# Kernel optimization log

Measured on AMD Instinct MI355X. Metric: run time of the kernel, lower is better.

The kernel has to match this reference:

```python
import jax, jax.numpy as jnp
import numpy as np

B, IN, H = 8192, 1024, 1024
WRANK, UR0, UR1, G = 256, 64, 32, 2
HG = H // G


def setup_inputs() -> dict:
    key = jax.random.key(0)
    ks = jax.random.split(key, 24)
    r = lambda k, shp: 0.1 * jax.random.normal(k, shp, dtype=jnp.float32)
    inp = {
        "x": jax.random.normal(ks[0], (B, IN), dtype=jnp.float32),
        "h": jax.random.normal(ks[1], (B, H), dtype=jnp.float32),
        "c": jax.random.normal(ks[2], (B, H), dtype=jnp.float32),
        "W": r(ks[3], (IN, WRANK)),
        "W1": r(ks[4], (WRANK, H)),
        "W2": r(ks[5], (WRANK, H)),
        "W3": r(ks[6], (WRANK, H)),
        "W4": r(ks[7], (WRANK, H)),
        "U": r(ks[8], (G, HG, UR0)),
        "U1": r(ks[9], (G, UR0, HG)),
        "U2": r(ks[10], (G, UR0, HG)),
        "U3": r(ks[11], (G, UR0, HG)),
        "U4": r(ks[12], (G, UR0, HG)),
        "UU": r(ks[13], (G, HG, UR1)),
        "UU1": r(ks[14], (G, UR1, HG)),
        "UU2": r(ks[15], (G, UR1, HG)),
        "UU3": r(ks[16], (G, UR1, HG)),
        "UU4": r(ks[17], (G, UR1, HG)),
        "bias_f": jnp.ones((1, H), dtype=jnp.float32),
        "bias_i": jnp.ones((1, H), dtype=jnp.float32),
        "bias_c": jnp.ones((1, H), dtype=jnp.float32),
        "bias_o": jnp.ones((1, H), dtype=jnp.float32),
    }
    return inp


def _grouped(hg, Ushare, Ui):
    # hg: [B, g, hg]; Ushare: [g, hg, r]; Ui: [g, r, hg] -> [B, H]
    t = jnp.einsum('bgd,gdr->bgr', hg, Ushare)
    return jnp.einsum('bgr,grd->bgd', t, Ui).reshape(hg.shape[0], H)


def reference(x, h, c, W, W1, W2, W3, W4, U, U1, U2, U3, U4,
              UU, UU1, UU2, UU3, UU4, bias_f, bias_i, bias_c, bias_o):
    # low-rank W path
    xw = x @ W                      # [B, wRank]
    wVal1, wVal2, wVal3, wVal4 = xw @ W1, xw @ W2, xw @ W3, xw @ W4

    # grouped low-rank U path (diagonal groups)
    hg = h.reshape(B, G, HG)
    tU = jnp.einsum('bgd,gdr->bgr', hg, U)          # shared projection
    uVal1 = jnp.einsum('bgr,grd->bgd', tU, U1).reshape(B, H)
    uVal2 = jnp.einsum('bgr,grd->bgd', tU, U2).reshape(B, H)
    uVal3 = jnp.einsum('bgr,grd->bgd', tU, U3).reshape(B, H)
    uVal4 = jnp.einsum('bgr,grd->bgd', tU, U4).reshape(B, H)

    # grouped UU path on group-rotated h (index = [1..g-1, 0])
    hg3 = jnp.roll(hg, -1, axis=1)
    tUU = jnp.einsum('bgd,gdr->bgr', hg3, UU)
    uuVal1 = jnp.einsum('bgr,grd->bgd', tUU, UU1).reshape(B, H)
    uuVal2 = jnp.einsum('bgr,grd->bgd', tUU, UU2).reshape(B, H)
    uuVal3 = jnp.einsum('bgr,grd->bgd', tUU, UU3).reshape(B, H)
    uuVal4 = jnp.einsum('bgr,grd->bgd', tUU, UU4).reshape(B, H)

    matVal_i = wVal1 + uVal1 + uuVal1
    matVal_f = wVal2 + uVal2 + uuVal2
    matVal_o = wVal3 + uVal3 + uuVal3
    matVal_c = wVal4 + uVal4 + uuVal4

    i = jax.nn.sigmoid(matVal_i + bias_i)
    f = jax.nn.sigmoid(matVal_f + bias_f)
    o = jax.nn.sigmoid(matVal_o + bias_o)
    c_tilda = jnp.tanh(matVal_c + bias_c)

    c_next = f * c + i * c_tilda
    h_next = o * jnp.tanh(c_next)
    return (c_next, h_next)
```

## Files before the change

kernel.cpp:

```cpp
#include <hip/hip_runtime.h>
#include <hip/hip_bf16.h>

#define B_ROWS 8192
#define IN_DIM 1024
#define H_DIM  1024
#define WRANK  256
#define UR0    64
#define UR1    32
#define HGD    512
#define KTOT   384
#define A2_LD  512

typedef __attribute__((ext_vector_type(8))) short bf16x8;
typedef __attribute__((ext_vector_type(4))) float f32x4;
typedef __attribute__((ext_vector_type(4))) float float4v;

__device__ __forceinline__ unsigned short f2bf(float f) {
    union { float f; unsigned u; } v; v.f = f;
    unsigned r = v.u + 0x7FFF + ((v.u >> 16) & 1);
    return (unsigned short)(r >> 16);
}

__device__ __forceinline__ void gld16(void* lds, const void* g) {
    __builtin_amdgcn_global_load_lds(
        (const __attribute__((address_space(1))) unsigned int*)g,
        (__attribute__((address_space(3))) unsigned int*)lds, 16, 0, 0);
}

__device__ __forceinline__ float fsig(float x)  { return 1.f / (1.f + __expf(-x)); }
__device__ __forceinline__ float ftanh(float x) { return 1.f - 2.f / (__expf(2.f * x) + 1.f); }

__global__ __launch_bounds__(256)
void pack_weights(const float* __restrict__ W,
                  const float* __restrict__ W1, const float* __restrict__ W2,
                  const float* __restrict__ W3, const float* __restrict__ W4,
                  const float* __restrict__ U,  const float* __restrict__ U1,
                  const float* __restrict__ U2, const float* __restrict__ U3,
                  const float* __restrict__ U4,
                  const float* __restrict__ UU, const float* __restrict__ UU1,
                  const float* __restrict__ UU2,const float* __restrict__ UU3,
                  const float* __restrict__ UU4,
                  unsigned short* __restrict__ WbfT,
                  unsigned short* __restrict__ HPbf,
                  unsigned short* __restrict__ GateBT)
{
    const float* Wg[4]  = {W1, W2, W3, W4};
    const float* Ug[4]  = {U1, U2, U3, U4};
    const float* UUg[4] = {UU1, UU2, UU3, UU4};
    const long N_WT = 256L * 1024;
    const long N_HP = 256L * 512;
    const long N_GB = 4L * 1024 * KTOT;
    const long total = N_WT + N_HP + N_GB;
    for (long t = blockIdx.x * 256L + threadIdx.x; t < total; t += (long)gridDim.x * 256L) {
        if (t < N_WT) {
            int n = (int)(t >> 10), p = (int)(t & 1023);
            int span = p >> 6, slp = (p >> 3) & 7, e = p & 7;
            int k = span * 64 + ((slp ^ (n & 7)) << 3) + e;
            WbfT[t] = f2bf(W[(size_t)k * WRANK + n]);
        } else if (t < N_WT + N_HP) {
            long u = t - N_WT;
            int n = (int)(u >> 9), p = (int)(u & 511);
            int span = p >> 6, slp = (p >> 3) & 7, e = p & 7;
            int k = span * 64 + ((slp ^ (n & 7)) << 3) + e;
            float v;
            if (n < 64)       v = U [(size_t)k * UR0 + n];
            else if (n < 96)  v = UU[(size_t)(HGD + k) * UR1 + (n - 64)];
            else if (n < 128) v = 0.f;
            else if (n < 192) v = U [(size_t)(HGD + k) * UR0 + (n - 128)];
            else if (n < 224) v = UU[(size_t)k * UR1 + (n - 192)];
            else              v = 0.f;
            HPbf[u] = f2bf(v);
        } else {
            long u = t - N_WT - N_HP;
            int q = (int)(u / (1024L * KTOT));
            long w = u - (long)q * 1024 * KTOT;
            int n = (int)(w / KTOT), p = (int)(w % KTOT);
            int span = p >> 6, slp = (p >> 3) & 7, e = p & 7;
            int k = span * 64 + ((slp ^ (n & 7)) << 3) + e;
            int g = n >> 9, nn = n & 511;
            float v;
            if (k < WRANK)            v = Wg[q][(size_t)k * H_DIM + n];
            else if (k < WRANK + UR0) v = Ug[q][((size_t)g * UR0 + (k - WRANK)) * HGD + nn];
            else if (k < 352)         v = UUg[q][((size_t)g * UR1 + (k - 320)) * HGD + nn];
            else                      v = 0.f;
            GateBT[u] = f2bf(v);
        }
    }
}

__global__ __launch_bounds__(256, 2)
void s1_kernel(const float* __restrict__ x, const float* __restrict__ h,
               const unsigned short* __restrict__ WbfT,
               const unsigned short* __restrict__ HPbf,
               unsigned short* __restrict__ A2)
{
    __shared__ short As[128 * 64];
    __shared__ short Bs[64 * 64];

    const int flat = blockIdx.x;
    const int id = (flat & 7) * 64 + (flat >> 3);
    const int bx = id & 7, by = id >> 3;
    const int m0 = by * 128;

    const bool pa = bx < 4;
    const int Kdim = pa ? IN_DIM : HGD;
    const float* Af = pa ? x : h;
    const int a_off = pa ? 0 : ((bx - 4) >> 1) * HGD;
    const unsigned short* Bw = pa ? (WbfT + (size_t)(bx * 64) * IN_DIM)
                                  : (HPbf + (size_t)((bx - 4) * 64) * HGD);
    const int ldbw = pa ? IN_DIM : HGD;
    const int ccol0 = pa ? bx * 64 : WRANK + (bx - 4) * 64;

    const int tid = threadIdx.x, lane = tid & 63, wid = tid >> 6;
    const int wr = wid >> 1, wc = wid & 1;
    const int lr = lane & 15, lh = lane >> 4;

    f32x4 acc[4][2];
    #pragma unroll
    for (int i = 0; i < 4; ++i)
        #pragma unroll
        for (int j = 0; j < 2; ++j) acc[i][j] = (f32x4){0.f, 0.f, 0.f, 0.f};

    for (int k0 = 0; k0 < Kdim; k0 += 64) {
        #pragma unroll
        for (int t = 0; t < 2; ++t) {
            int u = wid + t * 4;
            const char* src = (const char*)Bw
                + ((size_t)(u * 8 + (lane >> 3)) * ldbw + k0) * 2 + (lane & 7) * 16;
            gld16((char*)Bs + u * 1024, src);
        }
        #pragma unroll
        for (int t = 0; t < 4; ++t) {
            int c = tid + t * 256;
            int row = c >> 3, slot = c & 7;
            const float* p = Af + (size_t)(m0 + row) * 1024 + a_off + k0 + slot * 8;
            float4v f0 = *(const float4v*)p, f1 = *(const float4v*)(p + 4);
            union { bf16x8 v; unsigned short s[8]; } uv;
            uv.s[0] = f2bf(f0.x); uv.s[1] = f2bf(f0.y);
            uv.s[2] = f2bf(f0.z); uv.s[3] = f2bf(f0.w);
            uv.s[4] = f2bf(f1.x); uv.s[5] = f2bf(f1.y);
            uv.s[6] = f2bf(f1.z); uv.s[7] = f2bf(f1.w);
            *(bf16x8*)((char*)As + row * 128 + ((slot ^ (row & 7)) << 4)) = uv.v;
        }
        __syncthreads();
        #pragma unroll
        for (int ks = 0; ks < 2; ++ks) {
            bf16x8 af[4];
            #pragma unroll
            for (int i = 0; i < 4; ++i) {
                int r = wr * 64 + i * 16 + lr;
                af[i] = *(const bf16x8*)((const char*)As + r * 128 + (((ks * 4 + lh) ^ (r & 7)) << 4));
            }
            #pragma unroll
            for (int j = 0; j < 2; ++j) {
                int r = wc * 32 + j * 16 + lr;
                bf16x8 rb = *(const bf16x8*)((const char*)Bs + r * 128 + (((ks * 4 + lh) ^ (r & 7)) << 4));
                #pragma unroll
                for (int i = 0; i < 4; ++i)
                    acc[i][j] = __builtin_amdgcn_mfma_f32_16x16x32_bf16(af[i], rb, acc[i][j], 0, 0, 0);
            }
        }
        __syncthreads();
    }

    #pragma unroll
    for (int i = 0; i < 4; ++i) {
        #pragma unroll
        for (int j = 0; j < 2; ++j) {
            int ncol = ccol0 + wc * 32 + j * 16 + lr;
            int span = ncol >> 6, sl = (ncol >> 3) & 7, e = ncol & 7;
            #pragma unroll
            for (int rr = 0; rr < 4; ++rr) {
                int brow = m0 + wr * 64 + i * 16 + lh * 4 + rr;
                int phys = span * 64 + ((sl ^ (brow & 7)) << 3) + e;
                A2[(size_t)brow * A2_LD + phys] = f2bf(acc[i][j][rr]);
            }
        }
    }
}

__global__ __launch_bounds__(512, 2)
void s2_kernel(const unsigned short* __restrict__ A2,
               const unsigned short* __restrict__ GateBT,
               const float* __restrict__ bias_f, const float* __restrict__ bias_i,
               const float* __restrict__ bias_c, const float* __restrict__ bias_o,
               const float* __restrict__ cin,
               float* __restrict__ cout, float* __restrict__ hout)
{
    __shared__ short As[2][256 * 64];
    __shared__ short Bs[2][4][64 * 64];

    const int flat = blockIdx.x;
    const int id = (flat & 7) * 64 + (flat >> 3);
    const int nt = id & 15, mt = id >> 4;
    const int m0 = mt * 256, n0 = nt * 64, g = n0 >> 9;

    const int tid = threadIdx.x, lane = tid & 63, wid = tid >> 6;
    const int wr = wid >> 1, wc = wid & 1;
    const int lr = lane & 15, lh = lane >> 4;
    const int l8 = lane >> 3, l7 = lane & 7;

    f32x4 acc[4][4][2];
    #pragma unroll
    for (int q = 0; q < 4; ++q)
        #pragma unroll
        for (int i = 0; i < 4; ++i)
            #pragma unroll
            for (int j = 0; j < 2; ++j) acc[q][i][j] = (f32x4){0.f, 0.f, 0.f, 0.f};

#define STAGE_S2(buf, s) do {                                                        \
    const int _ms = ((s) < 4) ? (s) : (((s) == 4) ? 4 + 2 * g : 5 + 2 * (g ^ 1));    \
    _Pragma("unroll")                                                                \
    for (int t = 0; t < 4; ++t) {                                                    \
        int u = wid * 4 + t;                                                         \
        gld16((char*)&As[buf][0] + u * 1024,                                         \
              (const char*)A2 + ((size_t)(m0 + u * 8 + l8) * A2_LD + _ms * 64) * 2   \
              + l7 * 16);                                                            \
    }                                                                                \
    _Pragma("unroll")                                                                \
    for (int t = 0; t < 4; ++t) {                                                    \
        int v = wid * 4 + t, q = v >> 3, uu = v & 7;                                 \
        gld16((char*)&Bs[buf][q][0] + uu * 1024,                                     \
              (const char*)GateBT + ((size_t)(q * 1024 + n0 + uu * 8 + l8) * KTOT    \
              + (s) * 64) * 2 + l7 * 16);                                            \
    } } while (0)

    STAGE_S2(0, 0);

    #pragma unroll
    for (int s = 0; s < 6; ++s) {
        const int cur = s & 1;
        if (s < 5) {
            STAGE_S2(cur ^ 1, s + 1);
            asm volatile("s_waitcnt vmcnt(8)" ::: "memory");
        } else {
            asm volatile("s_waitcnt vmcnt(0)" ::: "memory");
        }
        __builtin_amdgcn_s_barrier();
        asm volatile("" ::: "memory");
        __builtin_amdgcn_s_setprio(1);
        #pragma unroll
        for (int ks = 0; ks < 2; ++ks) {
            bf16x8 af[4];
            #pragma unroll
            for (int i = 0; i < 4; ++i) {
                int r = wr * 64 + i * 16 + lr;
                af[i] = *(const bf16x8*)((const char*)&As[cur][0] + r * 128
                        + (((ks * 4 + lh) ^ (r & 7)) << 4));
            }
            #pragma unroll
            for (int q = 0; q < 4; ++q) {
                #pragma unroll
                for (int j = 0; j < 2; ++j) {
                    int r = wc * 32 + j * 16 + lr;
                    bf16x8 rb = *(const bf16x8*)((const char*)&Bs[cur][q][0] + r * 128
                                + (((ks * 4 + lh) ^ (r & 7)) << 4));
                    #pragma unroll
                    for (int i = 0; i < 4; ++i)
                        acc[q][i][j] = __builtin_amdgcn_mfma_f32_16x16x32_bf16(
                            af[i], rb, acc[q][i][j], 0, 0, 0);
                }
            }
        }
        __builtin_amdgcn_s_setprio(0);
        asm volatile("" ::: "memory");
        __builtin_amdgcn_s_barrier();
        asm volatile("" ::: "memory");
    }
#undef STAGE_S2

    #pragma unroll
    for (int j = 0; j < 2; ++j) {
        int ncol = n0 + wc * 32 + j * 16 + lr;
        float Bi = bias_i[ncol], Bf = bias_f[ncol];
        float Bo = bias_o[ncol], Bc = bias_c[ncol];
        #pragma unroll
        for (int i = 0; i < 4; ++i) {
            #pragma unroll
            for (int rr = 0; rr < 4; ++rr) {
                int brow = m0 + wr * 64 + i * 16 + lh * 4 + rr;
                float mi = acc[0][i][j][rr] + Bi;
                float mf = acc[1][i][j][rr] + Bf;
                float mo = acc[2][i][j][rr] + Bo;
                float mc = acc[3][i][j][rr] + Bc;
                float iv = fsig(mi), fv = fsig(mf), ov = fsig(mo);
                float ct = ftanh(mc);
                float cv = cin[(size_t)brow * H_DIM + ncol];
                float cn = fv * cv + iv * ct;
                float hn = ov * ftanh(cn);
                cout[(size_t)brow * H_DIM + ncol] = cn;
                hout[(size_t)brow * H_DIM + ncol] = hn;
            }
        }
    }
}

extern "C" void kernel_launch(void* const* d_in, const int* in_sizes, int n_in,
                              void* d_out, int out_size, void* d_ws, size_t ws_size,
                              hipStream_t stream)
{
    const float* x   = (const float*)d_in[0];
    const float* h   = (const float*)d_in[1];
    const float* c   = (const float*)d_in[2];
    const float* W   = (const float*)d_in[3];
    const float* W1  = (const float*)d_in[4];
    const float* W2  = (const float*)d_in[5];
    const float* W3  = (const float*)d_in[6];
    const float* W4  = (const float*)d_in[7];
    const float* U   = (const float*)d_in[8];
    const float* U1  = (const float*)d_in[9];
    const float* U2  = (const float*)d_in[10];
    const float* U3  = (const float*)d_in[11];
    const float* U4  = (const float*)d_in[12];
    const float* UU  = (const float*)d_in[13];
    const float* UU1 = (const float*)d_in[14];
    const float* UU2 = (const float*)d_in[15];
    const float* UU3 = (const float*)d_in[16];
    const float* UU4 = (const float*)d_in[17];
    const float* bias_f = (const float*)d_in[18];
    const float* bias_i = (const float*)d_in[19];
    const float* bias_c = (const float*)d_in[20];
    const float* bias_o = (const float*)d_in[21];

    unsigned short* A2     = (unsigned short*)d_ws;
    unsigned short* WbfT   = A2   + (size_t)B_ROWS * A2_LD;
    unsigned short* HPbf   = WbfT + 256L * 1024;
    unsigned short* GateBT = HPbf + 256L * 512;

    float* c_out = (float*)d_out;
    float* h_out = c_out + (size_t)B_ROWS * H_DIM;

    pack_weights<<<dim3(2048), dim3(256), 0, stream>>>(
        W, W1, W2, W3, W4, U, U1, U2, U3, U4, UU, UU1, UU2, UU3, UU4,
        WbfT, HPbf, GateBT);

    s1_kernel<<<dim3(512), dim3(256), 0, stream>>>(x, h, WbfT, HPbf, A2);

    s2_kernel<<<dim3(512), dim3(512), 0, stream>>>(
        A2, GateBT, bias_f, bias_i, bias_c, bias_o, c, c_out, h_out);
}
```

Baseline: 94.00 us.

## Retile both GEMM stages with pre-tiled intermediate layouts and pipelined loads

Stage one now uses 64-row tiles with double-buffered B loads and register-prefetched A, and writes its output in a tiled per-slab layout that drops the unused zero-padding columns. Stage two reads 32-wide K slabs from pre-tiled A and gate weight images, so each wave copies contiguous 1KB chunks with no swizzle math. The K depth shrinks from 384 padded to 352, and tile sizes drop so twice as many blocks run with higher occupancy. The cost is more blocks, more barriers per unit of K, and more complex index mapping that is easy to get wrong.

```diff
diff --git a/kernel.cpp b/kernel.cpp
--- a/kernel.cpp
+++ b/kernel.cpp
@@ -8,8 +8,9 @@
 #define UR0    64
 #define UR1    32
 #define HGD    512
-#define KTOT   384
-#define A2_LD  512
+
+#define NS2    11
+#define NTA    14
 
 typedef __attribute__((ext_vector_type(8))) short bf16x8;
 typedef __attribute__((ext_vector_type(4))) float f32x4;
@@ -42,15 +43,15 @@
                   const float* __restrict__ UU4,
                   unsigned short* __restrict__ WbfT,
                   unsigned short* __restrict__ HPbf,
-                  unsigned short* __restrict__ GateBT)
+                  unsigned short* __restrict__ BT2)
 {
     const float* Wg[4]  = {W1, W2, W3, W4};
     const float* Ug[4]  = {U1, U2, U3, U4};
     const float* UUg[4] = {UU1, UU2, UU3, UU4};
     const long N_WT = 256L * 1024;
     const long N_HP = 256L * 512;
-    const long N_GB = 4L * 1024 * KTOT;
-    const long total = N_WT + N_HP + N_GB;
+    const long N_BT = 16L * NS2 * 8192;
+    const long total = N_WT + N_HP + N_BT;
     for (long t = blockIdx.x * 256L + threadIdx.x; t < total; t += (long)gridDim.x * 256L) {
         if (t < N_WT) {
             int n = (int)(t >> 10), p = (int)(t & 1023);
@@ -72,35 +73,34 @@
             HPbf[u] = f2bf(v);
         } else {
             long u = t - N_WT - N_HP;
-            int q = (int)(u / (1024L * KTOT));
-            long w = u - (long)q * 1024 * KTOT;
-            int n = (int)(w / KTOT), p = (int)(w % KTOT);
-            int span = p >> 6, slp = (p >> 3) & 7, e = p & 7;
-            int k = span * 64 + ((slp ^ (n & 7)) << 3) + e;
-            int g = n >> 9, nn = n & 511;
+            int img = (int)(u >> 13);
+            int nt = img / NS2, s = img % NS2;
+            int r = (int)(u & 8191);
+            int q = r >> 11, kc = (r >> 9) & 3, row = (r >> 3) & 63, e = r & 7;
+            int n = nt * 64 + row, g = n >> 9, nn = n & 511;
+            int kk = kc * 8 + e;
             float v;
-            if (k < WRANK)            v = Wg[q][(size_t)k * H_DIM + n];
-            else if (k < WRANK + UR0) v = Ug[q][((size_t)g * UR0 + (k - WRANK)) * HGD + nn];
-            else if (k < 352)         v = UUg[q][((size_t)g * UR1 + (k - 320)) * HGD + nn];
-            else                      v = 0.f;
-            GateBT[u] = f2bf(v);
-        }
-    }
-}
-
-__global__ __launch_bounds__(256, 2)
+            if (s < 8)       v = Wg[q][(size_t)(s * 32 + kk) * H_DIM + n];
+            else if (s < 10) v = Ug[q][((size_t)g * UR0 + (s - 8) * 32 + kk) * HGD + nn];
+            else             v = UUg[q][((size_t)g * UR1 + kk) * HGD + nn];
+            BT2[u] = f2bf(v);
+        }
+    }
+}
+
+__global__ __launch_bounds__(256, 4)
 void s1_kernel(const float* __restrict__ x, const float* __restrict__ h,
                const unsigned short* __restrict__ WbfT,
                const unsigned short* __restrict__ HPbf,
-               unsigned short* __restrict__ A2)
+               unsigned short* __restrict__ A2T)
 {
-    __shared__ short As[128 * 64];
-    __shared__ short Bs[64 * 64];
+    __shared__ short As[64 * 64];
+    __shared__ short Bs[2][64 * 64];
 
     const int flat = blockIdx.x;
-    const int id = (flat & 7) * 64 + (flat >> 3);
+    const int id = (flat & 7) * 128 + (flat >> 3);
     const int bx = id & 7, by = id >> 3;
-    const int m0 = by * 128;
+    const int m0 = by * 64;
 
     const bool pa = bx < 4;
     const int Kdim = pa ? IN_DIM : HGD;
@@ -114,183 +114,211 @@
     const int tid = threadIdx.x, lane = tid & 63, wid = tid >> 6;
     const int wr = wid >> 1, wc = wid & 1;
     const int lr = lane & 15, lh = lane >> 4;
-
-    f32x4 acc[4][2];
-    #pragma unroll
-    for (int i = 0; i < 4; ++i)
+    const int l8 = lane >> 3, l7 = lane & 7;
+
+    f32x4 acc[2][2];
+    #pragma unroll
+    for (int i = 0; i < 2; ++i)
         #pragma unroll
         for (int j = 0; j < 2; ++j) acc[i][j] = (f32x4){0.f, 0.f, 0.f, 0.f};
 
-    for (int k0 = 0; k0 < Kdim; k0 += 64) {
-        #pragma unroll
-        for (int t = 0; t < 2; ++t) {
-            int u = wid + t * 4;
-            const char* src = (const char*)Bw
-                + ((size_t)(u * 8 + (lane >> 3)) * ldbw + k0) * 2 + (lane & 7) * 16;
-            gld16((char*)Bs + u * 1024, src);
-        }
-        #pragma unroll
-        for (int t = 0; t < 4; ++t) {
-            int c = tid + t * 256;
-            int row = c >> 3, slot = c & 7;
-            const float* p = Af + (size_t)(m0 + row) * 1024 + a_off + k0 + slot * 8;
-            float4v f0 = *(const float4v*)p, f1 = *(const float4v*)(p + 4);
-            union { bf16x8 v; unsigned short s[8]; } uv;
-            uv.s[0] = f2bf(f0.x); uv.s[1] = f2bf(f0.y);
-            uv.s[2] = f2bf(f0.z); uv.s[3] = f2bf(f0.w);
-            uv.s[4] = f2bf(f1.x); uv.s[5] = f2bf(f1.y);
-            uv.s[6] = f2bf(f1.z); uv.s[7] = f2bf(f1.w);
-            *(bf16x8*)((char*)As + row * 128 + ((slot ^ (row & 7)) << 4)) = uv.v;
-        }
-        __syncthreads();
+    float4v areg[2][2][2];
+
+#define S1_STAGEB(buf, kk) do {                                                   \
+    _Pragma("unroll")                                                             \
+    for (int t = 0; t < 2; ++t) {                                                 \
+        int u = wid * 2 + t;                                                      \
+        gld16((char*)&Bs[buf][0] + u * 1024,                                      \
+              (const char*)Bw + ((size_t)(u * 8 + l8) * ldbw + (kk)) * 2 + l7 * 16); \
+    } } while (0)
+
+#define S1_LOADA(set, kk) do {                                                    \
+    _Pragma("unroll")                                                             \
+    for (int t = 0; t < 2; ++t) {                                                 \
+        int cc = tid + t * 256;                                                   \
+        int row = cc >> 3, slot = cc & 7;                                         \
+        const float* p = Af + (size_t)(m0 + row) * 1024 + a_off + (kk) + slot * 8;\
+        areg[set][t][0] = *(const float4v*)p;                                     \
+        areg[set][t][1] = *(const float4v*)(p + 4);                               \
+    } } while (0)
+
+#define S1_WRITEA(set) do {                                                       \
+    _Pragma("unroll")                                                             \
+    for (int t = 0; t < 2; ++t) {                                                 \
+        int cc = tid + t * 256;                                                   \
+        int row = cc >> 3, slot = cc & 7;                                         \
+        union { bf16x8 v; unsigned short s_[8]; } uv;                             \
+        uv.s_[0] = f2bf(areg[set][t][0].x); uv.s_[1] = f2bf(areg[set][t][0].y);   \
+        uv.s_[2] = f2bf(areg[set][t][0].z); uv.s_[3] = f2bf(areg[set][t][0].w);   \
+        uv.s_[4] = f2bf(areg[set][t][1].x); uv.s_[5] = f2bf(areg[set][t][1].y);   \
+        uv.s_[6] = f2bf(areg[set][t][1].z); uv.s_[7] = f2bf(areg[set][t][1].w);   \
+        *(bf16x8*)((char*)As + row * 128 + ((slot ^ (row & 7)) << 4)) = uv.v;     \
+    } } while (0)
+
+    S1_STAGEB(0, 0);
+    S1_LOADA(0, 0);
+
+    #pragma unroll
+    for (int ki = 0; ki < 16; ++ki) {
+        if (ki * 64 >= Kdim) break;
+        const int cur = ki & 1;
+        const bool more = (ki + 1) * 64 < Kdim;
+        if (more) S1_STAGEB(cur ^ 1, (ki + 1) * 64);
+        if (more) { asm volatile("s_waitcnt vmcnt(2)" ::: "memory"); }
+        else      { asm volatile("s_waitcnt vmcnt(0)" ::: "memory"); }
+        S1_WRITEA(cur);
+        if (more) S1_LOADA(cur ^ 1, (ki + 1) * 64);
+        asm volatile("s_waitcnt lgkmcnt(0)" ::: "memory");
+        __builtin_amdgcn_s_barrier();
+        asm volatile("" ::: "memory");
         #pragma unroll
         for (int ks = 0; ks < 2; ++ks) {
-            bf16x8 af[4];
-            #pragma unroll
-            for (int i = 0; i < 4; ++i) {
-                int r = wr * 64 + i * 16 + lr;
-                af[i] = *(const bf16x8*)((const char*)As + r * 128 + (((ks * 4 + lh) ^ (r & 7)) << 4));
+            bf16x8 af[2];
+            #pragma unroll
+            for (int i = 0; i < 2; ++i) {
+                int r = wr * 32 + i * 16 + lr;
+                af[i] = *(const bf16x8*)((const char*)As + r * 128
+                        + (((ks * 4 + lh) ^ (r & 7)) << 4));
             }
             #pragma unroll
             for (int j = 0; j < 2; ++j) {
                 int r = wc * 32 + j * 16 + lr;
-                bf16x8 rb = *(const bf16x8*)((const char*)Bs + r * 128 + (((ks * 4 + lh) ^ (r & 7)) << 4));
+                bf16x8 rb = *(const bf16x8*)((const char*)&Bs[cur][0] + r * 128
+                            + (((ks * 4 + lh) ^ (r & 7)) << 4));
                 #pragma unroll
-                for (int i = 0; i < 4; ++i)
-                    acc[i][j] = __builtin_amdgcn_mfma_f32_16x16x32_bf16(af[i], rb, acc[i][j], 0, 0, 0);
+                for (int i = 0; i < 2; ++i)
+                    acc[i][j] = __builtin_amdgcn_mfma_f32_16x16x32_bf16(
+                        af[i], rb, acc[i][j], 0, 0, 0);
             }
         }
-        __syncthreads();
-    }
-
-    #pragma unroll
-    for (int i = 0; i < 4; ++i) {
+        asm volatile("" ::: "memory");
+        __builtin_amdgcn_s_barrier();
+        asm volatile("" ::: "memory");
+    }
+#undef S1_STAGEB
+#undef S1_LOADA
+#undef S1_WRITEA
+
+    #pragma unroll
+    for (int i = 0; i < 2; ++i) {
         #pragma unroll
         for (int j = 0; j < 2; ++j) {
             int ncol = ccol0 + wc * 32 + j * 16 + lr;
-            int span = ncol >> 6, sl = (ncol >> 3) & 7, e = ncol & 7;
+            int blk = ncol >> 5;
+            if (blk == 11 || blk == 15) continue;
+            int tt = (blk <= 10) ? blk : blk - 1;
+            int kk = ncol & 31, kc = kk >> 3, e = kk & 7;
             #pragma unroll
             for (int rr = 0; rr < 4; ++rr) {
-                int brow = m0 + wr * 64 + i * 16 + lh * 4 + rr;
-                int phys = span * 64 + ((sl ^ (brow & 7)) << 3) + e;
-                A2[(size_t)brow * A2_LD + phys] = f2bf(acc[i][j][rr]);
+                int brow = m0 + wr * 32 + i * 16 + lh * 4 + rr;
+                A2T[((size_t)(brow >> 8) * NTA + tt) * 8192 + kc * 2048
+                    + (brow & 255) * 8 + e] = f2bf(acc[i][j][rr]);
             }
         }
     }
 }
 
-__global__ __launch_bounds__(512, 2)
-void s2_kernel(const unsigned short* __restrict__ A2,
-               const unsigned short* __restrict__ GateBT,
+__global__ __launch_bounds__(512, 4)
+void s2_kernel(const unsigned short* __restrict__ A2T,
+               const unsigned short* __restrict__ BT2,
                const float* __restrict__ bias_f, const float* __restrict__ bias_i,
                const float* __restrict__ bias_c, const float* __restrict__ bias_o,
                const float* __restrict__ cin,
                float* __restrict__ cout, float* __restrict__ hout)
 {
-    __shared__ short As[2][256 * 64];
-    __shared__ short Bs[2][4][64 * 64];
+    __shared__ short As[2][128 * 32];
+    __shared__ short Bs[2][4 * 64 * 32];
 
     const int flat = blockIdx.x;
-    const int id = (flat & 7) * 64 + (flat >> 3);
+    const int id = (flat & 7) * 128 + (flat >> 3);
     const int nt = id & 15, mt = id >> 4;
-    const int m0 = mt * 256, n0 = nt * 64, g = n0 >> 9;
+    const int m0 = mt * 128, n0 = nt * 64, g = nt >> 3;
 
     const int tid = threadIdx.x, lane = tid & 63, wid = tid >> 6;
-    const int wr = wid >> 1, wc = wid & 1;
+    const int wr = wid >> 2, wc = wid & 3;
     const int lr = lane & 15, lh = lane >> 4;
-    const int l8 = lane >> 3, l7 = lane & 7;
-
-    f32x4 acc[4][4][2];
+
+    const char* Abase = (const char*)A2T + (size_t)(mt >> 1) * NTA * 16384
+                        + (mt & 1) * 2048 + (wid >> 1) * 4096 + (wid & 1) * 1024
+                        + lane * 16;
+    const char* Bbase = (const char*)BT2 + (size_t)nt * NS2 * 16384 + lane * 16;
+
+    f32x4 acc[4][4];
     #pragma unroll
     for (int q = 0; q < 4; ++q)
         #pragma unroll
-        for (int i = 0; i < 4; ++i)
-            #pragma unroll
-            for (int j = 0; j < 2; ++j) acc[q][i][j] = (f32x4){0.f, 0.f, 0.f, 0.f};
-
-#define STAGE_S2(buf, s) do {                                                        \
-    const int _ms = ((s) < 4) ? (s) : (((s) == 4) ? 4 + 2 * g : 5 + 2 * (g ^ 1));    \
-    _Pragma("unroll")                                                                \
-    for (int t = 0; t < 4; ++t) {                                                    \
-        int u = wid * 4 + t;                                                         \
-        gld16((char*)&As[buf][0] + u * 1024,                                         \
-              (const char*)A2 + ((size_t)(m0 + u * 8 + l8) * A2_LD + _ms * 64) * 2   \
-              + l7 * 16);                                                            \
-    }                                                                                \
-    _Pragma("unroll")                                                                \
-    for (int t = 0; t < 4; ++t) {                                                    \
-        int v = wid * 4 + t, q = v >> 3, uu = v & 7;                                 \
-        gld16((char*)&Bs[buf][q][0] + uu * 1024,                                     \
-              (const char*)GateBT + ((size_t)(q * 1024 + n0 + uu * 8 + l8) * KTOT    \
-              + (s) * 64) * 2 + l7 * 16);                                            \
+        for (int i = 0; i < 4; ++i) acc[q][i] = (f32x4){0.f, 0.f, 0.f, 0.f};
+
+#define S2_TA(s) ((s) < 8 ? (s) : (g == 0 ? ((s) == 10 ? 13 : (s)) \
+                                          : ((s) == 10 ? 10 : (s) + 3)))
+#define S2_STAGE(buf, s, tA) do {                                                 \
+    gld16((char*)&As[buf][0] + wid * 1024, Abase + (size_t)(tA) * 16384);         \
+    _Pragma("unroll")                                                             \
+    for (int t = 0; t < 2; ++t) {                                                 \
+        int u = wid * 2 + t;                                                      \
+        gld16((char*)&Bs[buf][0] + u * 1024,                                      \
+              Bbase + (size_t)(s) * 16384 + u * 1024);                            \
     } } while (0)
 
-    STAGE_S2(0, 0);
-
-    #pragma unroll
-    for (int s = 0; s < 6; ++s) {
+    S2_STAGE(0, 0, 0);
+
+    #pragma unroll
+    for (int s = 0; s < NS2; ++s) {
         const int cur = s & 1;
-        if (s < 5) {
-            STAGE_S2(cur ^ 1, s + 1);
-            asm volatile("s_waitcnt vmcnt(8)" ::: "memory");
+        if (s < NS2 - 1) {
+            const int sn = s + 1;
+            const int tA = S2_TA(sn);
+            S2_STAGE(cur ^ 1, sn, tA);
+            asm volatile("s_waitcnt vmcnt(3)" ::: "memory");
         } else {
             asm volatile("s_waitcnt vmcnt(0)" ::: "memory");
         }
         __builtin_amdgcn_s_barrier();
         asm volatile("" ::: "memory");
         __builtin_amdgcn_s_setprio(1);
-        #pragma unroll
-        for (int ks = 0; ks < 2; ++ks) {
+        {
             bf16x8 af[4];
             #pragma unroll
-            for (int i = 0; i < 4; ++i) {
-                int r = wr * 64 + i * 16 + lr;
-                af[i] = *(const bf16x8*)((const char*)&As[cur][0] + r * 128
-                        + (((ks * 4 + lh) ^ (r & 7)) << 4));
+            for (int i = 0; i < 4; ++i)
+                af[i] = *(const bf16x8*)((const char*)&As[cur][0]
+                        + lh * 2048 + (wr * 64 + i * 16 + lr) * 16);
+            #pragma unroll
+            for (int q = 0; q < 4; ++q) {
+                bf16x8 rb = *(const bf16x8*)((const char*)&Bs[cur][0]
+                            + q * 4096 + lh * 1024 + (wc * 16 + lr) * 16);
+                #pragma unroll
+                for (int i = 0; i < 4; ++i)
+                    acc[q][i] = __builtin_amdgcn_mfma_f32_16x16x32_bf16(
+                        af[i], rb, acc[q][i], 0, 0, 0);
             }
-            #pragma unroll
-            for (int q = 0; q < 4; ++q) {
-                #pragma unroll
-                for (int j = 0; j < 2; ++j) {
-                    int r = wc * 32 + j * 16 + lr;
-                    bf16x8 rb = *(const bf16x8*)((const char*)&Bs[cur][q][0] + r * 128
-                                + (((ks * 4 + lh) ^ (r & 7)) << 4));
-                    #pragma unroll
-                    for (int i = 0; i < 4; ++i)
-                        acc[q][i][j] = __builtin_amdgcn_mfma_f32_16x16x32_bf16(
-                            af[i], rb, acc[q][i][j], 0, 0, 0);
-                }
-            }
         }
         __builtin_amdgcn_s_setprio(0);
         asm volatile("" ::: "memory");
         __builtin_amdgcn_s_barrier();
         asm volatile("" ::: "memory");
     }
-#undef STAGE_S2
-
-    #pragma unroll
-    for (int j = 0; j < 2; ++j) {
-        int ncol = n0 + wc * 32 + j * 16 + lr;
-        float Bi = bias_i[ncol], Bf = bias_f[ncol];
-        float Bo = bias_o[ncol], Bc = bias_c[ncol];
-        #pragma unroll
-        for (int i = 0; i < 4; ++i) {
-            #pragma unroll
-            for (int rr = 0; rr < 4; ++rr) {
-                int brow = m0 + wr * 64 + i * 16 + lh * 4 + rr;
-                float mi = acc[0][i][j][rr] + Bi;
-                float mf = acc[1][i][j][rr] + Bf;
-                float mo = acc[2][i][j][rr] + Bo;
-                float mc = acc[3][i][j][rr] + Bc;
-                float iv = fsig(mi), fv = fsig(mf), ov = fsig(mo);
-                float ct = ftanh(mc);
-                float cv = cin[(size_t)brow * H_DIM + ncol];
-                float cn = fv * cv + iv * ct;
-                float hn = ov * ftanh(cn);
-                cout[(size_t)brow * H_DIM + ncol] = cn;
-                hout[(size_t)brow * H_DIM + ncol] = hn;
-            }
+#undef S2_STAGE
+#undef S2_TA
+
+    const int ncol = n0 + wc * 16 + lr;
+    const float Bi = bias_i[ncol], Bf = bias_f[ncol];
+    const float Bo = bias_o[ncol], Bc = bias_c[ncol];
+    #pragma unroll
+    for (int i = 0; i < 4; ++i) {
+        #pragma unroll
+        for (int rr = 0; rr < 4; ++rr) {
+            int brow = m0 + wr * 64 + i * 16 + lh * 4 + rr;
+            float mi = acc[0][i][rr] + Bi;
+            float mf = acc[1][i][rr] + Bf;
+            float mo = acc[2][i][rr] + Bo;
+            float mc = acc[3][i][rr] + Bc;
+            float iv = fsig(mi), fv = fsig(mf), ov = fsig(mo);
+            float ct = ftanh(mc);
+            float cv = cin[(size_t)brow * H_DIM + ncol];
+            float cn = fv * cv + iv * ct;
+            float hn = ov * ftanh(cn);
+            cout[(size_t)brow * H_DIM + ncol] = cn;
+            hout[(size_t)brow * H_DIM + ncol] = hn;
         }
     }
 }
@@ -322,20 +350,20 @@
     const float* bias_c = (const float*)d_in[20];
     const float* bias_o = (const float*)d_in[21];
 
-    unsigned short* A2     = (unsigned short*)d_ws;
-    unsigned short* WbfT   = A2   + (size_t)B_ROWS * A2_LD;
-    unsigned short* HPbf   = WbfT + 256L * 1024;
-    unsigned short* GateBT = HPbf + 256L * 512;
+    unsigned short* A2T  = (unsigned short*)d_ws;
+    unsigned short* WbfT = A2T  + 32L * NTA * 8192;
+    unsigned short* HPbf = WbfT + 256L * 1024;
+    unsigned short* BT2  = HPbf + 256L * 512;
 
     float* c_out = (float*)d_out;
     float* h_out = c_out + (size_t)B_ROWS * H_DIM;
 
     pack_weights<<<dim3(2048), dim3(256), 0, stream>>>(
         W, W1, W2, W3, W4, U, U1, U2, U3, U4, UU, UU1, UU2, UU3, UU4,
-        WbfT, HPbf, GateBT);
-
-    s1_kernel<<<dim3(512), dim3(256), 0, stream>>>(x, h, WbfT, HPbf, A2);
-
-    s2_kernel<<<dim3(512), dim3(512), 0, stream>>>(
-        A2, GateBT, bias_f, bias_i, bias_c, bias_o, c, c_out, h_out);
-}
+        WbfT, HPbf, BT2);
+
+    s1_kernel<<<dim3(1024), dim3(256), 0, stream>>>(x, h, WbfT, HPbf, A2T);
+
+    s2_kernel<<<dim3(1024), dim3(512), 0, stream>>>(
+        A2T, BT2, bias_f, bias_i, bias_c, bias_o, c, c_out, h_out);
+}
```

After: 84.22 us. 1.12x faster.
